# Kernel tuning notes

Hardware: AMD Instinct MI355X
Metric: run time of the kernel (lower is better)

## Reference

```python
import jax, jax.numpy as jnp
import numpy as np

N = 500000   # total nodes
C = 128      # input_features
R = 4        # reduction
B = 32       # batch_num (graphs)


def setup_inputs() -> dict:
    key = jax.random.key(0)
    k0, k1, k2, k3, k4, k5 = jax.random.split(key, 6)
    x_input = jax.random.normal(k0, (N, C), dtype=jnp.float32)
    batch = jnp.sort(jax.random.randint(k1, (N,), 0, B)).astype(jnp.int64)
    # SE gate MLP params: Linear(C, C//R) -> ReLU -> Linear(C//R, C)
    W1 = jax.random.normal(k2, (C, C // R), dtype=jnp.float32) * (1.0 / np.sqrt(C))
    b1 = jax.random.normal(k3, (C // R,), dtype=jnp.float32) * 0.01
    W2 = jax.random.normal(k4, (C // R, C), dtype=jnp.float32) * (1.0 / np.sqrt(C // R))
    b2 = jax.random.normal(k5, (C,), dtype=jnp.float32) * 0.01
    return {"x_input": x_input, "batch": batch, "batch_num": B,
            "W1": W1, "b1": b1, "W2": W2, "b2": b2}


def reference(x_input, batch, batch_num, W1, b1, W2, b2):
    # segment mean pool over graphs (global_mean_pool)
    sums = jax.ops.segment_sum(x_input, batch, num_segments=batch_num)          # [B, C]
    counts = jax.ops.segment_sum(jnp.ones((x_input.shape[0],), x_input.dtype),
                                 batch, num_segments=batch_num)                  # [B]
    avg = sums / jnp.maximum(counts, 1.0)[:, None]
    # 2-layer MLP gate + sigmoid
    h = jax.nn.relu(avg @ W1 + b1)
    attn = jax.nn.sigmoid(h @ W2 + b2)                                           # [B, C]
    # per-node broadcast multiply (gather attn by graph id)
    return x_input * attn[batch]
```

## Files before the change

kernel.cpp:

```cpp
#include <hip/hip_runtime.h>
#include <hip/hip_bf16.h>

#define C 128
#define CR 32
#define B 32
#define RPB 128

typedef float f32x4 __attribute__((ext_vector_type(4)));

__device__ inline int lower_bound_i(const int* __restrict__ a, int n, int key) {
    int lo = 0, hi = n;
    while (lo < hi) {
        int mid = (lo + hi) >> 1;
        if (a[mid] < key) lo = mid + 1; else hi = mid;
    }
    return lo;
}

__global__ __launch_bounds__(256, 8) void seg_partial_kernel(
    const f32x4* __restrict__ x4, const int* __restrict__ batch,
    f32x4* __restrict__ partial4, int N)
{
    const int t  = threadIdx.x;
    const int c4 = t & 31;
    const int rl = t >> 5;
    const long base = (long)blockIdx.x * RPB;
    long rend = base + RPB;
    if (rend > N) rend = N;

    if (batch[base] != batch[rend - 1]) return;

    const f32x4* p = x4 + (base + rl) * 32 + c4;
    long r = base + rl;
    f32x4 a0 = (f32x4)(0.f), a1 = (f32x4)(0.f);
    f32x4 a2 = (f32x4)(0.f), a3 = (f32x4)(0.f);
    while (r + 56 < rend) {
        f32x4 v0 = p[0 * 256];
        f32x4 v1 = p[1 * 256];
        f32x4 v2 = p[2 * 256];
        f32x4 v3 = p[3 * 256];
        f32x4 v4 = p[4 * 256];
        f32x4 v5 = p[5 * 256];
        f32x4 v6 = p[6 * 256];
        f32x4 v7 = p[7 * 256];
        a0 += v0; a1 += v1; a2 += v2; a3 += v3;
        a0 += v4; a1 += v5; a2 += v6; a3 += v7;
        r += 64; p += 8 * 256;
    }
    while (r < rend) { a0 += p[0]; r += 8; p += 256; }
    f32x4 acc = (a0 + a1) + (a2 + a3);

    __shared__ f32x4 s_red[8][32];
    s_red[rl][c4] = acc;
    __syncthreads();
    if (t < 32) {
        f32x4 s = s_red[0][t];
        #pragma unroll
        for (int i = 1; i < 8; ++i) s += s_red[i][t];
        partial4[(long)blockIdx.x * 32 + t] = s;
    }
}

__global__ __launch_bounds__(1024) void reduce_mlp_kernel(
    const f32x4* __restrict__ x4, const int* __restrict__ batch,
    const f32x4* __restrict__ partial4,
    const float* __restrict__ W1, const float* __restrict__ b1,
    const float* __restrict__ W2, const float* __restrict__ b2,
    float* __restrict__ attn, int N)
{
    const int seg = blockIdx.x;
    const int t   = threadIdx.x;
    const int c4  = t & 31;
    const int rl  = t >> 5;

    const int lo = lower_bound_i(batch, N, seg);
    const int hi = lower_bound_i(batch, N, seg + 1);

    f32x4 acc = (f32x4)(0.f);
    const int fb0 = (lo + RPB - 1) / RPB;
    const int fb1 = hi / RPB;
    if (fb0 < fb1) {
        for (int blk = fb0 + rl; blk < fb1; blk += 32)
            acc += partial4[(long)blk * 32 + c4];
        #pragma unroll 4
        for (long r = lo + rl; r < (long)fb0 * RPB; r += 32)
            acc += x4[r * 32 + c4];
        #pragma unroll 4
        for (long r = (long)fb1 * RPB + rl; r < hi; r += 32)
            acc += x4[r * 32 + c4];
    } else {
        #pragma unroll 4
        for (long r = lo + rl; r < hi; r += 32)
            acc += x4[r * 32 + c4];
    }

    __shared__ f32x4 s_red[32][32];
    __shared__ float s_avg[C];
    __shared__ float s_h[CR];
    s_red[rl][c4] = acc;
    __syncthreads();
    if (t < 32) {
        f32x4 s = s_red[0][t];
        #pragma unroll
        for (int i = 1; i < 32; ++i) s += s_red[i][t];
        float inv = 1.0f / fmaxf((float)(hi - lo), 1.0f);
        s_avg[4 * t + 0] = s.x * inv;
        s_avg[4 * t + 1] = s.y * inv;
        s_avg[4 * t + 2] = s.z * inv;
        s_avg[4 * t + 3] = s.w * inv;
    }
    __syncthreads();
    if (t < CR) {
        float d = b1[t];
        #pragma unroll 8
        for (int c = 0; c < C; ++c)
            d += s_avg[c] * W1[c * CR + t];
        s_h[t] = fmaxf(d, 0.f);
    }
    __syncthreads();
    if (t < C) {
        float d = b2[t];
        #pragma unroll
        for (int j = 0; j < CR; ++j)
            d += s_h[j] * W2[j * C + t];
        attn[seg * C + t] = 1.0f / (1.0f + expf(-d));
    }
}

__global__ __launch_bounds__(256, 8) void scale_kernel(
    const f32x4* __restrict__ x4, const int* __restrict__ batch,
    const f32x4* __restrict__ attn4, f32x4* __restrict__ out4,
    long total4)
{
    long idx    = (long)blockIdx.x * blockDim.x + threadIdx.x;
    long stride = (long)gridDim.x * blockDim.x;
    for (; idx < total4; idx += stride) {
        long row = idx >> 5;
        int  c4  = (int)(idx & 31);
        int  b   = batch[row];
        f32x4 o = x4[idx] * attn4[b * 32 + c4];
        __builtin_nontemporal_store(o, &out4[idx]);
    }
}

extern "C" void kernel_launch(void* const* d_in, const int* in_sizes, int n_in,
                              void* d_out, int out_size, void* d_ws, size_t ws_size,
                              hipStream_t stream) {
    const float* x     = (const float*)d_in[0];
    const int*   batch = (const int*)d_in[1];
    const float* W1 = (const float*)d_in[3];
    const float* b1 = (const float*)d_in[4];
    const float* W2 = (const float*)d_in[5];
    const float* b2 = (const float*)d_in[6];
    float* out = (float*)d_out;

    const int N = in_sizes[0] / C;
    const int ntiles = (N + RPB - 1) / RPB;

    float* attn    = (float*)d_ws;
    float* partial = attn + B * C;

    seg_partial_kernel<<<ntiles, 256, 0, stream>>>((const f32x4*)x, batch,
                                                   (f32x4*)partial, N);

    reduce_mlp_kernel<<<B, 1024, 0, stream>>>((const f32x4*)x, batch,
                                              (const f32x4*)partial,
                                              W1, b1, W2, b2, attn, N);

    const long total4 = (long)N * 32;
    scale_kernel<<<4096, 256, 0, stream>>>((const f32x4*)x, batch,
                                           (const f32x4*)attn, (f32x4*)out,
                                           total4);
}
```

Measured before the change: 136.3 us.

## Fuse gate MLP into scale kernel and handle boundary tiles in partial pass

The partial-sum kernel now uses larger 1024-row tiles with 512 threads. Tiles that straddle a segment boundary are split at the boundary and emit two partial sums, so the reduction no longer rereads raw rows. The separate reduce/MLP kernel is removed: every block of the new gate_scale kernel redundantly reduces the per-tile partials for all 32 segments, runs the MLP into shared memory, and then does the broadcast multiply from shared attention. This saves a kernel launch and the serial 32-block reduce stage. In exchange, each of the 1024 blocks repeats the gate computation and the W1/W2 reads, and the boundary logic assumes a tile spans at most two segments.

```diff
diff --git a/kernel.cpp b/kernel.cpp
--- a/kernel.cpp
+++ b/kernel.cpp
@@ -1,10 +1,9 @@
 #include <hip/hip_runtime.h>
-#include <hip/hip_bf16.h>
 
 #define C 128
 #define CR 32
 #define B 32
-#define RPB 128
+#define RPB 1024
 
 typedef float f32x4 __attribute__((ext_vector_type(4)));
 
@@ -17,7 +16,7 @@
     return lo;
 }
 
-__global__ __launch_bounds__(256, 8) void seg_partial_kernel(
+__global__ __launch_bounds__(512, 4) void seg_partial_kernel(
     const f32x4* __restrict__ x4, const int* __restrict__ batch,
     f32x4* __restrict__ partial4, int N)
 {
@@ -27,118 +26,144 @@
     const long base = (long)blockIdx.x * RPB;
     long rend = base + RPB;
     if (rend > N) rend = N;
+    const int segA = batch[base];
+    const int segB = batch[rend - 1];
 
-    if (batch[base] != batch[rend - 1]) return;
+    __shared__ f32x4 s_redA[16][32];
+    __shared__ f32x4 s_redB[16][32];
 
-    const f32x4* p = x4 + (base + rl) * 32 + c4;
-    long r = base + rl;
-    f32x4 a0 = (f32x4)(0.f), a1 = (f32x4)(0.f);
-    f32x4 a2 = (f32x4)(0.f), a3 = (f32x4)(0.f);
-    while (r + 56 < rend) {
-        f32x4 v0 = p[0 * 256];
-        f32x4 v1 = p[1 * 256];
-        f32x4 v2 = p[2 * 256];
-        f32x4 v3 = p[3 * 256];
-        f32x4 v4 = p[4 * 256];
-        f32x4 v5 = p[5 * 256];
-        f32x4 v6 = p[6 * 256];
-        f32x4 v7 = p[7 * 256];
-        a0 += v0; a1 += v1; a2 += v2; a3 += v3;
-        a0 += v4; a1 += v5; a2 += v6; a3 += v7;
-        r += 64; p += 8 * 256;
-    }
-    while (r < rend) { a0 += p[0]; r += 8; p += 256; }
-    f32x4 acc = (a0 + a1) + (a2 + a3);
+    if (segA == segB) {
+        const f32x4* p = x4 + (base + rl) * 32 + c4;
+        long r = base + rl;
+        f32x4 a0 = (f32x4)(0.f), a1 = (f32x4)(0.f);
+        f32x4 a2 = (f32x4)(0.f), a3 = (f32x4)(0.f);
+        while (r + 112 < rend) {
+            f32x4 v0 = p[0 * 512];
+            f32x4 v1 = p[1 * 512];
+            f32x4 v2 = p[2 * 512];
+            f32x4 v3 = p[3 * 512];
+            f32x4 v4 = p[4 * 512];
+            f32x4 v5 = p[5 * 512];
+            f32x4 v6 = p[6 * 512];
+            f32x4 v7 = p[7 * 512];
+            a0 += v0; a1 += v1; a2 += v2; a3 += v3;
+            a0 += v4; a1 += v5; a2 += v6; a3 += v7;
+            r += 128; p += 8 * 512;
+        }
+        while (r < rend) { a0 += p[0]; r += 16; p += 512; }
+        f32x4 acc = (a0 + a1) + (a2 + a3);
 
-    __shared__ f32x4 s_red[8][32];
-    s_red[rl][c4] = acc;
-    __syncthreads();
-    if (t < 32) {
-        f32x4 s = s_red[0][t];
-        #pragma unroll
-        for (int i = 1; i < 8; ++i) s += s_red[i][t];
-        partial4[(long)blockIdx.x * 32 + t] = s;
+        s_redA[rl][c4] = acc;
+        __syncthreads();
+        if (t < 32) {
+            f32x4 s = s_redA[0][t];
+            #pragma unroll
+            for (int i = 1; i < 16; ++i) s += s_redA[i][t];
+            partial4[(long)blockIdx.x * 64 + t] = s;
+        }
+    } else {
+        long mlo = base, mhi = rend - 1;
+        while (mlo < mhi) {
+            long mid = (mlo + mhi) >> 1;
+            if (batch[mid] < segB) mlo = mid + 1; else mhi = mid;
+        }
+        const long m = mlo;
+
+        f32x4 aA = (f32x4)(0.f), aB = (f32x4)(0.f);
+        for (long r = base + rl; r < m; r += 16)
+            aA += x4[r * 32 + c4];
+        for (long r = m + rl; r < rend; r += 16)
+            aB += x4[r * 32 + c4];
+
+        s_redA[rl][c4] = aA;
+        s_redB[rl][c4] = aB;
+        __syncthreads();
+        if (t < 32) {
+            f32x4 sA = s_redA[0][t], sB = s_redB[0][t];
+            #pragma unroll
+            for (int i = 1; i < 16; ++i) { sA += s_redA[i][t]; sB += s_redB[i][t]; }
+            partial4[(long)blockIdx.x * 64 + t]      = sA;
+            partial4[(long)blockIdx.x * 64 + 32 + t] = sB;
+        }
     }
 }
 
-__global__ __launch_bounds__(1024) void reduce_mlp_kernel(
+__global__ __launch_bounds__(256, 8) void gate_scale_kernel(
     const f32x4* __restrict__ x4, const int* __restrict__ batch,
     const f32x4* __restrict__ partial4,
     const float* __restrict__ W1, const float* __restrict__ b1,
     const float* __restrict__ W2, const float* __restrict__ b2,
-    float* __restrict__ attn, int N)
+    f32x4* __restrict__ out4, int N)
 {
-    const int seg = blockIdx.x;
-    const int t   = threadIdx.x;
-    const int c4  = t & 31;
-    const int rl  = t >> 5;
+    const int t  = threadIdx.x;
+    const int c4 = t & 31;
+    const int sl = t >> 5;
 
-    const int lo = lower_bound_i(batch, N, seg);
-    const int hi = lower_bound_i(batch, N, seg + 1);
+    __shared__ int   s_bnd[B + 1];
+    __shared__ f32x4 s_buf4[B][32];
+    __shared__ float s_h[B][CR];
+    float* s_buf = (float*)s_buf4;
 
-    f32x4 acc = (f32x4)(0.f);
-    const int fb0 = (lo + RPB - 1) / RPB;
-    const int fb1 = hi / RPB;
-    if (fb0 < fb1) {
-        for (int blk = fb0 + rl; blk < fb1; blk += 32)
-            acc += partial4[(long)blk * 32 + c4];
-        #pragma unroll 4
-        for (long r = lo + rl; r < (long)fb0 * RPB; r += 32)
-            acc += x4[r * 32 + c4];
-        #pragma unroll 4
-        for (long r = (long)fb1 * RPB + rl; r < hi; r += 32)
-            acc += x4[r * 32 + c4];
-    } else {
-        #pragma unroll 4
-        for (long r = lo + rl; r < hi; r += 32)
-            acc += x4[r * 32 + c4];
-    }
+    if (t <= B) s_bnd[t] = lower_bound_i(batch, N, t);
+    __syncthreads();
 
-    __shared__ f32x4 s_red[32][32];
-    __shared__ float s_avg[C];
-    __shared__ float s_h[CR];
-    s_red[rl][c4] = acc;
-    __syncthreads();
-    if (t < 32) {
-        f32x4 s = s_red[0][t];
-        #pragma unroll
-        for (int i = 1; i < 32; ++i) s += s_red[i][t];
-        float inv = 1.0f / fmaxf((float)(hi - lo), 1.0f);
-        s_avg[4 * t + 0] = s.x * inv;
-        s_avg[4 * t + 1] = s.y * inv;
-        s_avg[4 * t + 2] = s.z * inv;
-        s_avg[4 * t + 3] = s.w * inv;
+    for (int s = sl; s < B; s += 8) {
+        const int lo = s_bnd[s], hi = s_bnd[s + 1];
+        f32x4 acc = (f32x4)(0.f);
+        if (lo < hi) {
+            const int t0 = lo / RPB;
+            const int t1 = (hi - 1) / RPB;
+            int tt = t0;
+            if ((lo % RPB) != 0) {
+                acc += partial4[(long)tt * 64 + 32 + c4];
+                ++tt;
+            }
+            for (; tt + 3 <= t1; tt += 4) {
+                f32x4 u0 = partial4[(long)(tt + 0) * 64 + c4];
+                f32x4 u1 = partial4[(long)(tt + 1) * 64 + c4];
+                f32x4 u2 = partial4[(long)(tt + 2) * 64 + c4];
+                f32x4 u3 = partial4[(long)(tt + 3) * 64 + c4];
+                acc += u0; acc += u1; acc += u2; acc += u3;
+            }
+            for (; tt <= t1; ++tt)
+                acc += partial4[(long)tt * 64 + c4];
+        }
+        const float inv = 1.0f / fmaxf((float)(hi - lo), 1.0f);
+        s_buf[s * C + c4 * 4 + 0] = acc.x * inv;
+        s_buf[s * C + c4 * 4 + 1] = acc.y * inv;
+        s_buf[s * C + c4 * 4 + 2] = acc.z * inv;
+        s_buf[s * C + c4 * 4 + 3] = acc.w * inv;
     }
     __syncthreads();
-    if (t < CR) {
-        float d = b1[t];
+
+    for (int k = t; k < B * CR; k += 256) {
+        int s = k >> 5, j = k & (CR - 1);
+        float d = b1[j];
         #pragma unroll 8
         for (int c = 0; c < C; ++c)
-            d += s_avg[c] * W1[c * CR + t];
-        s_h[t] = fmaxf(d, 0.f);
+            d += s_buf[s * C + c] * W1[c * CR + j];
+        s_h[s][j] = fmaxf(d, 0.f);
     }
     __syncthreads();
-    if (t < C) {
-        float d = b2[t];
+
+    for (int k = t; k < B * C; k += 256) {
+        int s = k >> 7, c = k & (C - 1);
+        float d = b2[c];
         #pragma unroll
         for (int j = 0; j < CR; ++j)
-            d += s_h[j] * W2[j * C + t];
-        attn[seg * C + t] = 1.0f / (1.0f + expf(-d));
+            d += s_h[s][j] * W2[j * C + c];
+        s_buf[s * C + c] = 1.0f / (1.0f + expf(-d));
     }
-}
+    __syncthreads();
 
-__global__ __launch_bounds__(256, 8) void scale_kernel(
-    const f32x4* __restrict__ x4, const int* __restrict__ batch,
-    const f32x4* __restrict__ attn4, f32x4* __restrict__ out4,
-    long total4)
-{
-    long idx    = (long)blockIdx.x * blockDim.x + threadIdx.x;
-    long stride = (long)gridDim.x * blockDim.x;
+    const long total4 = (long)N * 32;
+    long idx = (long)blockIdx.x * 256 + t;
+    const long stride = (long)gridDim.x * 256;
     for (; idx < total4; idx += stride) {
         long row = idx >> 5;
-        int  c4  = (int)(idx & 31);
+        int  cc  = (int)(idx & 31);
         int  b   = batch[row];
-        f32x4 o = x4[idx] * attn4[b * 32 + c4];
+        f32x4 o = x4[idx] * s_buf4[b][cc];
         __builtin_nontemporal_store(o, &out4[idx]);
     }
 }
@@ -157,18 +182,13 @@
     const int N = in_sizes[0] / C;
     const int ntiles = (N + RPB - 1) / RPB;
 
-    float* attn    = (float*)d_ws;
-    float* partial = attn + B * C;
+    f32x4* partial = (f32x4*)d_ws;
 
-    seg_partial_kernel<<<ntiles, 256, 0, stream>>>((const f32x4*)x, batch,
-                                                   (f32x4*)partial, N);
+    seg_partial_kernel<<<ntiles, 512, 0, stream>>>((const f32x4*)x, batch,
+                                                   partial, N);
 
-    reduce_mlp_kernel<<<B, 1024, 0, stream>>>((const f32x4*)x, batch,
-                                              (const f32x4*)partial,
-                                              W1, b1, W2, b2, attn, N);
-
-    const long total4 = (long)N * 32;
-    scale_kernel<<<4096, 256, 0, stream>>>((const f32x4*)x, batch,
-                                           (const f32x4*)attn, (f32x4*)out,
-                                           total4);
+    gate_scale_kernel<<<1024, 256, 0, stream>>>((const f32x4*)x, batch,
+                                                (const f32x4*)partial,
+                                                W1, b1, W2, b2,
+                                                (f32x4*)out, N);
 }
```

Measured after the change: 166.0 us. 21.9% more time.
